# Kernel optimization log

Hardware: AMD Instinct MI355X
Metric: run time of the kernel (lower is better)

Reference implementation:

```python
import jax, jax.numpy as jnp
import numpy as np

B, N, F, C, K = 4, 8192, 128, 64, 16


def setup_inputs() -> dict:
    key = jax.random.key(0)
    ks = jax.random.split(key, 24)
    s = 0.05
    rn = lambda k, shape: (jax.random.normal(k, shape, jnp.float32) * s)
    return {
        "features": jax.random.normal(ks[0], (B, N, F), jnp.float32),
        "positions": jax.random.normal(ks[1], (B, N, 3), jnp.float32),
        "batch": jnp.repeat(jnp.arange(B, dtype=jnp.int32), N),
        "num_neighbors": K,
        # linear encoder (F -> C)
        "W_enc": rn(ks[2], (F, C)), "b_enc": jnp.zeros((C,), jnp.float32),
        # point-transformer q/k/v projections (C -> C)
        "Wq": rn(ks[3], (C, C)), "bq": jnp.zeros((C,), jnp.float32),
        "Wk": rn(ks[4], (C, C)), "bk": jnp.zeros((C,), jnp.float32),
        "Wv": rn(ks[5], (C, C)), "bv": jnp.zeros((C,), jnp.float32),
        # positional encoding MLP: 3 -> C -> C (ReLU)
        "Wp1": rn(ks[6], (3, C)), "bp1": jnp.zeros((C,), jnp.float32),
        "Wp2": rn(ks[7], (C, C)), "bp2": jnp.zeros((C,), jnp.float32),
        # attention MLP gamma: C -> C -> C (ReLU)
        "Wa1": rn(ks[8], (C, C)), "ba1": jnp.zeros((C,), jnp.float32),
        "Wa2": rn(ks[9], (C, C)), "ba2": jnp.zeros((C,), jnp.float32),
        # linear decoder (C -> F)
        "W_dec": rn(ks[10], (C, F)), "b_dec": jnp.zeros((F,), jnp.float32),
    }


def reference(features, positions, batch, num_neighbors,
              W_enc, b_enc, Wq, bq, Wk, bk, Wv, bv,
              Wp1, bp1, Wp2, bp2, Wa1, ba1, Wa2, ba2, W_dec, b_dec):
    # linear encode: [B,N,F] -> [B,N,C]
    x = features @ W_enc + b_enc
    q = x @ Wq + bq
    k = x @ Wk + bk
    v = x @ Wv + bv

    def per_cloud(pos, qi, ki, vi):
        # kNN via pairwise squared distances (self included, dist 0)
        sq = jnp.sum(pos * pos, axis=-1)                      # [N]
        d2 = sq[:, None] + sq[None, :] - 2.0 * (pos @ pos.T)  # [N,N]
        idx = jax.lax.top_k(-d2, num_neighbors)[1]            # [N,K]
        kj = ki[idx]                                          # [N,K,C] gather
        vj = vi[idx]                                          # [N,K,C]
        rel = pos[:, None, :] - pos[idx]                      # [N,K,3]
        # positional encoding delta = MLP(p_i - p_j)
        delta = jax.nn.relu(rel @ Wp1 + bp1) @ Wp2 + bp2      # [N,K,C]
        # vector attention: gamma(q_i - k_j + delta), softmax over K neighbors
        a = qi[:, None, :] - kj + delta
        a = jax.nn.relu(a @ Wa1 + ba1) @ Wa2 + ba2
        w = jax.nn.softmax(a, axis=1)                         # [N,K,C]
        return jnp.sum(w * (vj + delta), axis=1)              # [N,C]

    y = jax.vmap(per_cloud)(positions, q, k, v)               # [B,N,C]
    out = y @ W_dec + b_dec + features                        # decode + residual
    return (out, positions, batch)
```

## Files before the change

### kernel.cpp

```cpp
#include <hip/hip_runtime.h>
#include <hip/hip_bf16.h>

#define NPTS 32768
#define NPC  8192
#define KNN  16
#define CH   64
#define FDIM 128
#define EMPTYKEY 0x7F7FFFFFu

typedef __bf16 bf16;
typedef __bf16 bf16x8 __attribute__((ext_vector_type(8)));
typedef float  f32x4  __attribute__((ext_vector_type(4)));

__global__ __launch_bounds__(256) void k_encode(
    const float* __restrict__ feat,
    const float* __restrict__ Wenc, const float* __restrict__ benc,
    const float* __restrict__ Wq, const float* __restrict__ bq,
    const float* __restrict__ Wk, const float* __restrict__ bk,
    const float* __restrict__ Wv, const float* __restrict__ bv,
    float* __restrict__ qo, float* __restrict__ ko, float* __restrict__ vo)
{
    __shared__ float xs[4][CH];
    int t = threadIdx.x;
    int c = t & 63, pl = t >> 6;
    size_t pt = (size_t)blockIdx.x * 4 + pl;
    const float* fr = feat + pt * FDIM;
    float acc = benc[c];
#pragma unroll 8
    for (int f4 = 0; f4 < 32; ++f4) {
        float4 fv = *reinterpret_cast<const float4*>(fr + f4 * 4);
        acc += fv.x * Wenc[(f4*4+0)*CH + c];
        acc += fv.y * Wenc[(f4*4+1)*CH + c];
        acc += fv.z * Wenc[(f4*4+2)*CH + c];
        acc += fv.w * Wenc[(f4*4+3)*CH + c];
    }
    xs[pl][c] = acc;
    __syncthreads();
    float aq = bq[c], ak = bk[c], av = bv[c];
#pragma unroll 4
    for (int m = 0; m < CH; ++m) {
        float xm = xs[pl][m];
        aq += xm * Wq[m*CH + c];
        ak += xm * Wk[m*CH + c];
        av += xm * Wv[m*CH + c];
    }
    qo[pt*CH + c] = aq; ko[pt*CH + c] = ak; vo[pt*CH + c] = av;
}

__global__ __launch_bounds__(256, 4) void k_knn(
    const float* __restrict__ pos, unsigned* __restrict__ wsK)
{
    __shared__ float4 sp[1024];
    __shared__ unsigned sbuf[256 * 17];

    int t = threadIdx.x;
    int blk = blockIdx.x;
    int slice = blk & 7;
    int qg = (blk >> 3) & 31;
    int cloud = blk >> 8;
    const float* pc = pos + (size_t)cloud * NPC * 3;
    int jbase = slice << 10;

#pragma unroll
    for (int i = 0; i < 4; ++i) {
        int li = t * 4 + i;
        int j = jbase + li;
        sp[li] = make_float4(pc[j*3+0], pc[j*3+1], pc[j*3+2], 0.f);
    }
    __syncthreads();

    int qi = (qg << 8) + t;
    float myx = pc[qi*3+0], myy = pc[qi*3+1], myz = pc[qi*3+2];

    unsigned arr[16];
#pragma unroll
    for (int r = 0; r < 16; ++r) arr[r] = EMPTYKEY;
    float thrf = __uint_as_float(EMPTYKEY & 0xFFFFE000u);
    int cnt = 0;
    int base = t * 17;

    for (int g = 0; g < 1024; g += 4) {
#pragma unroll
        for (int u = 0; u < 4; ++u) {
            float4 p = sp[g + u];
            float dx = myx - p.x, dy = myy - p.y, dz = myz - p.z;
            float d2 = dx*dx + dy*dy + dz*dz;
            unsigned key = (__float_as_uint(d2) & 0xFFFFE000u) | (unsigned)(jbase + g + u);
            sbuf[base + cnt] = key;
            cnt += (d2 <= thrf) ? 1 : 0;
        }
        if (__any(cnt >= 13)) {
#pragma unroll
            for (int b = 0; b < 16; ++b) {
                unsigned key = (b < cnt) ? sbuf[base + b] : EMPTYKEY;
#pragma unroll
                for (int r = 0; r < 16; ++r) {
                    unsigned lo = key < arr[r] ? key : arr[r];
                    unsigned hi = key < arr[r] ? arr[r] : key;
                    arr[r] = lo; key = hi;
                }
            }
            cnt = 0;
            thrf = __uint_as_float(arr[15] & 0xFFFFE000u);
        }
    }
#pragma unroll
    for (int b = 0; b < 16; ++b) {
        unsigned key = (b < cnt) ? sbuf[base + b] : EMPTYKEY;
#pragma unroll
        for (int r = 0; r < 16; ++r) {
            unsigned lo = key < arr[r] ? key : arr[r];
            unsigned hi = key < arr[r] ? arr[r] : key;
            arr[r] = lo; key = hi;
        }
    }
    unsigned* o = wsK + (((size_t)(cloud * NPC + qi)) * 8 + slice) * 16;
#pragma unroll
    for (int r = 0; r < 16; ++r) o[r] = arr[r];
}

__global__ __launch_bounds__(64) void k_merge(
    const unsigned* __restrict__ wsK, int* __restrict__ idxout)
{
    __shared__ unsigned kk[64][137];
    int t = threadIdx.x;
    size_t q = (size_t)blockIdx.x * 64 + t;
    const uint4* src = reinterpret_cast<const uint4*>(wsK + q * 128);
#pragma unroll
    for (int i = 0; i < 32; ++i) {
        uint4 v = src[i];
        int w = i * 4;
        int s = (w >> 4) * 17 + (w & 15);
        kk[t][s] = v.x; kk[t][s+1] = v.y; kk[t][s+2] = v.z; kk[t][s+3] = v.w;
    }
#pragma unroll
    for (int l = 0; l < 8; ++l) kk[t][l*17 + 16] = 0xFFFFFFFFu;

    unsigned h0=0,h1=0,h2=0,h3=0,h4=0,h5=0,h6=0,h7=0;
    int* o = idxout + q * KNN;
    for (int r = 0; r < KNN; ++r) {
        unsigned best = 0xFFFFFFFFu; int bl = 0; unsigned k;
        k = kk[t][0*17 + h0]; if (k < best) { best = k; bl = 0; }
        k = kk[t][1*17 + h1]; if (k < best) { best = k; bl = 1; }
        k = kk[t][2*17 + h2]; if (k < best) { best = k; bl = 2; }
        k = kk[t][3*17 + h3]; if (k < best) { best = k; bl = 3; }
        k = kk[t][4*17 + h4]; if (k < best) { best = k; bl = 4; }
        k = kk[t][5*17 + h5]; if (k < best) { best = k; bl = 5; }
        k = kk[t][6*17 + h6]; if (k < best) { best = k; bl = 6; }
        k = kk[t][7*17 + h7]; if (k < best) { best = k; bl = 7; }
        o[r] = (int)(best & 0x1FFFu);
        h0 += (bl == 0); h1 += (bl == 1); h2 += (bl == 2); h3 += (bl == 3);
        h4 += (bl == 4); h5 += (bl == 5); h6 += (bl == 6); h7 += (bl == 7);
    }
}

__device__ __forceinline__ void wave_gemm(
    const bf16* At, f32x4 acc[4][4], const float* __restrict__ Wg,
    int w, int mlane, int kgrp)
{
    bf16x8 wf[4][2];
#pragma unroll
    for (int nt = 0; nt < 4; ++nt) {
#pragma unroll
        for (int kt = 0; kt < 2; ++kt) {
            bf16x8 v;
#pragma unroll
            for (int j = 0; j < 8; ++j)
                v[j] = (bf16)Wg[(kt*32 + kgrp*8 + j)*CH + nt*16 + mlane];
            wf[nt][kt] = v;
        }
    }
#pragma unroll
    for (int mt = 0; mt < 4; ++mt) {
        int row = w*64 + mt*16 + mlane;
        const bf16* rb = At + row*CH;
        int sw = row & 7;
        bf16x8 a0 = *reinterpret_cast<const bf16x8*>(rb + ((kgrp     ^ sw) * 8));
        bf16x8 a1 = *reinterpret_cast<const bf16x8*>(rb + (((4+kgrp) ^ sw) * 8));
#pragma unroll
        for (int nt = 0; nt < 4; ++nt) {
            acc[mt][nt] = __builtin_amdgcn_mfma_f32_16x16x32_bf16(a0, wf[nt][0], acc[mt][nt], 0, 0, 0);
            acc[mt][nt] = __builtin_amdgcn_mfma_f32_16x16x32_bf16(a1, wf[nt][1], acc[mt][nt], 0, 0, 0);
        }
    }
}

__global__ __launch_bounds__(128) void k_attn(
    const float* __restrict__ pos, const int* __restrict__ nidx,
    const float* __restrict__ qg, const float* __restrict__ kg, const float* __restrict__ vg,
    const float* __restrict__ Wp1, const float* __restrict__ bp1,
    const float* __restrict__ Wp2, const float* __restrict__ bp2,
    const float* __restrict__ Wa1, const float* __restrict__ ba1,
    const float* __restrict__ Wa2, const float* __restrict__ ba2,
    float* __restrict__ yout)
{
    __shared__ bf16 At[128 * CH];
    __shared__ bf16 Vt[128 * CH];

    int t = threadIdx.x;
    int w = t >> 6, lane = t & 63;
    int mlane = lane & 15, kgrp = lane >> 4;
    size_t p0 = (size_t)blockIdx.x * 8;
    size_t cbase = (p0 >> 13) << 13;

    {
        int p = t >> 4, j = t & 15;
        size_t gp = p0 + p;
        int nbr = nidx[gp*KNN + j];
        size_t gn = cbase + (size_t)nbr;
        float rx = pos[gp*3+0] - pos[gn*3+0];
        float ry = pos[gp*3+1] - pos[gn*3+1];
        float rz = pos[gp*3+2] - pos[gn*3+2];
        float h[CH];
#pragma unroll
        for (int c4 = 0; c4 < 16; ++c4) {
            float4 w0 = *reinterpret_cast<const float4*>(Wp1 + 0*CH + c4*4);
            float4 w1 = *reinterpret_cast<const float4*>(Wp1 + 1*CH + c4*4);
            float4 w2 = *reinterpret_cast<const float4*>(Wp1 + 2*CH + c4*4);
            float4 bb = *reinterpret_cast<const float4*>(bp1 + c4*4);
            h[c4*4+0] = fmaxf(rx*w0.x + ry*w1.x + rz*w2.x + bb.x, 0.f);
            h[c4*4+1] = fmaxf(rx*w0.y + ry*w1.y + rz*w2.y + bb.y, 0.f);
            h[c4*4+2] = fmaxf(rx*w0.z + ry*w1.z + rz*w2.z + bb.z, 0.f);
            h[c4*4+3] = fmaxf(rx*w0.w + ry*w1.w + rz*w2.w + bb.w, 0.f);
        }
#pragma unroll
        for (int ch = 0; ch < 8; ++ch) {
            bf16x8 v;
#pragma unroll
            for (int e = 0; e < 8; ++e) v[e] = (bf16)h[ch*8 + e];
            *reinterpret_cast<bf16x8*>(&At[t*CH + (ch ^ (t & 7)) * 8]) = v;
        }
    }

    f32x4 acc[4][4];

#pragma unroll
    for (int nt = 0; nt < 4; ++nt) {
        float b = bp2[nt*16 + mlane];
#pragma unroll
        for (int mt = 0; mt < 4; ++mt) { acc[mt][nt][0]=b; acc[mt][nt][1]=b; acc[mt][nt][2]=b; acc[mt][nt][3]=b; }
    }
    wave_gemm(At, acc, Wp2, w, mlane, kgrp);

#pragma unroll
    for (int mt = 0; mt < 4; ++mt) {
        size_t gp = p0 + (size_t)(w*4 + mt);
        int nb[4];
#pragma unroll
        for (int reg = 0; reg < 4; ++reg)
            nb[reg] = nidx[gp*KNN + kgrp*4 + reg];
#pragma unroll
        for (int nt = 0; nt < 4; ++nt) {
            int c = nt*16 + mlane;
            float qv = qg[gp*CH + c];
#pragma unroll
            for (int reg = 0; reg < 4; ++reg) {
                float dlt = acc[mt][nt][reg];
                size_t gr = cbase + (size_t)nb[reg];
                float kv = kg[gr*CH + c];
                float vv = vg[gr*CH + c];
                int row = w*64 + mt*16 + kgrp*4 + reg;
                int off = row*CH + (((c >> 3) ^ (row & 7)) * 8) + (c & 7);
                At[off] = (bf16)(qv - kv + dlt);
                Vt[off] = (bf16)(vv + dlt);
            }
        }
    }

#pragma unroll
    for (int nt = 0; nt < 4; ++nt) {
        float b = ba1[nt*16 + mlane];
#pragma unroll
        for (int mt = 0; mt < 4; ++mt) { acc[mt][nt][0]=b; acc[mt][nt][1]=b; acc[mt][nt][2]=b; acc[mt][nt][3]=b; }
    }
    wave_gemm(At, acc, Wa1, w, mlane, kgrp);
#pragma unroll
    for (int mt = 0; mt < 4; ++mt) {
#pragma unroll
        for (int nt = 0; nt < 4; ++nt) {
            int c = nt*16 + mlane;
#pragma unroll
            for (int reg = 0; reg < 4; ++reg) {
                int row = w*64 + mt*16 + kgrp*4 + reg;
                int off = row*CH + (((c >> 3) ^ (row & 7)) * 8) + (c & 7);
                At[off] = (bf16)fmaxf(acc[mt][nt][reg], 0.f);
            }
        }
    }

#pragma unroll
    for (int nt = 0; nt < 4; ++nt) {
        float b = ba2[nt*16 + mlane];
#pragma unroll
        for (int mt = 0; mt < 4; ++mt) { acc[mt][nt][0]=b; acc[mt][nt][1]=b; acc[mt][nt][2]=b; acc[mt][nt][3]=b; }
    }
    wave_gemm(At, acc, Wa2, w, mlane, kgrp);

#pragma unroll
    for (int mt = 0; mt < 4; ++mt) {
        size_t gp = p0 + (size_t)(w*4 + mt);
#pragma unroll
        for (int nt = 0; nt < 4; ++nt) {
            int c = nt*16 + mlane;
            float m = fmaxf(fmaxf(acc[mt][nt][0], acc[mt][nt][1]),
                            fmaxf(acc[mt][nt][2], acc[mt][nt][3]));
            m = fmaxf(m, __shfl_xor(m, 16));
            m = fmaxf(m, __shfl_xor(m, 32));
            float e[4], s = 0.f;
#pragma unroll
            for (int reg = 0; reg < 4; ++reg) { e[reg] = __expf(acc[mt][nt][reg] - m); s += e[reg]; }
            s += __shfl_xor(s, 16);
            s += __shfl_xor(s, 32);
            float num = 0.f;
#pragma unroll
            for (int reg = 0; reg < 4; ++reg) {
                int row = w*64 + mt*16 + kgrp*4 + reg;
                int off = row*CH + (((c >> 3) ^ (row & 7)) * 8) + (c & 7);
                num += e[reg] * (float)Vt[off];
            }
            num += __shfl_xor(num, 16);
            num += __shfl_xor(num, 32);
            if (kgrp == 0) yout[gp*CH + c] = num / s;
        }
    }
}

__global__ __launch_bounds__(256) void k_decode(
    const float* __restrict__ y, const float* __restrict__ Wd, const float* __restrict__ bd,
    const float* __restrict__ feat, float* __restrict__ out)
{
    int t = threadIdx.x;
    int f = t & 127, pl = t >> 7;
    size_t pt = (size_t)blockIdx.x * 2 + pl;
    const float* yr = y + pt*CH;
    float acc = bd[f] + feat[pt*FDIM + f];
#pragma unroll
    for (int c4 = 0; c4 < 16; ++c4) {
        float4 yv = *reinterpret_cast<const float4*>(yr + c4*4);
        acc += yv.x * Wd[(c4*4+0)*FDIM + f];
        acc += yv.y * Wd[(c4*4+1)*FDIM + f];
        acc += yv.z * Wd[(c4*4+2)*FDIM + f];
        acc += yv.w * Wd[(c4*4+3)*FDIM + f];
    }
    out[pt*FDIM + f] = acc;
}

__global__ void k_tail(const float* __restrict__ pos, const int* __restrict__ batch,
                       float* __restrict__ outtail)
{
    int i = blockIdx.x * 256 + threadIdx.x;
    if (i < NPTS*3) outtail[i] = pos[i];
    if (i < NPTS)   outtail[NPTS*3 + i] = (float)batch[i];
}

extern "C" void kernel_launch(void* const* d_in, const int* in_sizes, int n_in,
                              void* d_out, int out_size, void* d_ws, size_t ws_size,
                              hipStream_t stream)
{
    const float* feat  = (const float*)d_in[0];
    const float* pos   = (const float*)d_in[1];
    const int*   batch = (const int*)d_in[2];
    const float* Wenc  = (const float*)d_in[4];
    const float* benc  = (const float*)d_in[5];
    const float* Wq = (const float*)d_in[6];   const float* bq = (const float*)d_in[7];
    const float* Wk = (const float*)d_in[8];   const float* bk = (const float*)d_in[9];
    const float* Wv = (const float*)d_in[10];  const float* bv = (const float*)d_in[11];
    const float* Wp1= (const float*)d_in[12];  const float* bp1= (const float*)d_in[13];
    const float* Wp2= (const float*)d_in[14];  const float* bp2= (const float*)d_in[15];
    const float* Wa1= (const float*)d_in[16];  const float* ba1= (const float*)d_in[17];
    const float* Wa2= (const float*)d_in[18];  const float* ba2= (const float*)d_in[19];
    const float* Wd = (const float*)d_in[20];  const float* bd = (const float*)d_in[21];
    float* out = (float*)d_out;

    int*      idx = (int*)d_ws;
    unsigned* wsK = (unsigned*)((char*)d_ws + (size_t)NPTS*KNN*sizeof(int));
    float* qb = (float*)wsK;
    float* kb = qb + (size_t)NPTS*CH;
    float* vb = kb + (size_t)NPTS*CH;
    float* yb = vb + (size_t)NPTS*CH;

    k_knn<<<1024, 256, 0, stream>>>(pos, wsK);
    k_merge<<<NPTS/64, 64, 0, stream>>>(wsK, idx);

    k_encode<<<NPTS/4, 256, 0, stream>>>(feat, Wenc, benc, Wq, bq, Wk, bk, Wv, bv, qb, kb, vb);

    k_attn<<<NPTS/8, 128, 0, stream>>>(pos, idx, qb, kb, vb,
                                       Wp1, bp1, Wp2, bp2, Wa1, ba1, Wa2, ba2, yb);

    k_decode<<<NPTS/2, 256, 0, stream>>>(yb, Wd, bd, feat, out);

    k_tail<<<(NPTS*3 + 255)/256, 256, 0, stream>>>(pos, batch, out + (size_t)NPTS*FDIM);
}
```

Before: 472.6 us.

## Skip kNN candidate writes for distant groups and prepack MFMA weights

In the kNN kernel, the four distances of a group are computed first, and the shared-buffer write and insertion sort only run when some lane has a candidate under the current threshold. This removes the per-point unconditional LDS store. Position loads into shared memory now use vectorized float4 reads. A new tiny k_pack kernel converts Wp2, Wa1 and Wa2 once into MFMA-ready bf16x8 fragments, so each attention block loads 8 vectors instead of doing 64 strided fp32 loads and conversions per GEMM. The cost is one extra launch and more branching in the kNN loop.

```diff
diff --git a/kernel.cpp b/kernel.cpp
--- a/kernel.cpp
+++ b/kernel.cpp
@@ -61,11 +61,13 @@
     const float* pc = pos + (size_t)cloud * NPC * 3;
     int jbase = slice << 10;
 
-#pragma unroll
-    for (int i = 0; i < 4; ++i) {
-        int li = t * 4 + i;
-        int j = jbase + li;
-        sp[li] = make_float4(pc[j*3+0], pc[j*3+1], pc[j*3+2], 0.f);
+    {
+        const float4* src = reinterpret_cast<const float4*>(pc + (size_t)jbase * 3);
+        float4 a = src[t*3+0], b1 = src[t*3+1], c1 = src[t*3+2];
+        sp[t*4+0] = make_float4(a.x,  a.y,  a.z,  0.f);
+        sp[t*4+1] = make_float4(a.w,  b1.x, b1.y, 0.f);
+        sp[t*4+2] = make_float4(b1.z, b1.w, c1.x, 0.f);
+        sp[t*4+3] = make_float4(c1.y, c1.z, c1.w, 0.f);
     }
     __syncthreads();
 
@@ -80,28 +82,37 @@
     int base = t * 17;
 
     for (int g = 0; g < 1024; g += 4) {
+        float d2v[4];
 #pragma unroll
         for (int u = 0; u < 4; ++u) {
             float4 p = sp[g + u];
             float dx = myx - p.x, dy = myy - p.y, dz = myz - p.z;
-            float d2 = dx*dx + dy*dy + dz*dz;
-            unsigned key = (__float_as_uint(d2) & 0xFFFFE000u) | (unsigned)(jbase + g + u);
-            sbuf[base + cnt] = key;
-            cnt += (d2 <= thrf) ? 1 : 0;
-        }
-        if (__any(cnt >= 13)) {
-#pragma unroll
-            for (int b = 0; b < 16; ++b) {
-                unsigned key = (b < cnt) ? sbuf[base + b] : EMPTYKEY;
-#pragma unroll
-                for (int r = 0; r < 16; ++r) {
-                    unsigned lo = key < arr[r] ? key : arr[r];
-                    unsigned hi = key < arr[r] ? arr[r] : key;
-                    arr[r] = lo; key = hi;
+            d2v[u] = dx*dx + dy*dy + dz*dz;
+        }
+        float m4 = fminf(fminf(d2v[0], d2v[1]), fminf(d2v[2], d2v[3]));
+        if (__any(m4 <= thrf)) {
+#pragma unroll
+            for (int u = 0; u < 4; ++u) {
+                if (d2v[u] <= thrf) {
+                    sbuf[base + cnt] = (__float_as_uint(d2v[u]) & 0xFFFFE000u)
+                                       | (unsigned)(jbase + g + u);
+                    ++cnt;
                 }
             }
-            cnt = 0;
-            thrf = __uint_as_float(arr[15] & 0xFFFFE000u);
+            if (__any(cnt >= 13)) {
+#pragma unroll
+                for (int b = 0; b < 16; ++b) {
+                    unsigned key = (b < cnt) ? sbuf[base + b] : EMPTYKEY;
+#pragma unroll
+                    for (int r = 0; r < 16; ++r) {
+                        unsigned lo = min(key, arr[r]);
+                        unsigned hi = max(key, arr[r]);
+                        arr[r] = lo; key = hi;
+                    }
+                }
+                cnt = 0;
+                thrf = __uint_as_float(arr[15] & 0xFFFFE000u);
+            }
         }
     }
 #pragma unroll
@@ -109,8 +120,8 @@
         unsigned key = (b < cnt) ? sbuf[base + b] : EMPTYKEY;
 #pragma unroll
         for (int r = 0; r < 16; ++r) {
-            unsigned lo = key < arr[r] ? key : arr[r];
-            unsigned hi = key < arr[r] ? arr[r] : key;
+            unsigned lo = min(key, arr[r]);
+            unsigned hi = max(key, arr[r]);
             arr[r] = lo; key = hi;
         }
     }
@@ -154,25 +165,43 @@
     }
 }
 
+__global__ __launch_bounds__(64) void k_pack(
+    const float* __restrict__ Wp2, const float* __restrict__ Wa1,
+    const float* __restrict__ Wa2, bf16* __restrict__ wpk)
+{
+    int lane = threadIdx.x;
+    int mlane = lane & 15, kgrp = lane >> 4;
+    const float* Ws[3] = {Wp2, Wa1, Wa2};
+    bf16x8* o = reinterpret_cast<bf16x8*>(wpk);
+    for (int gmm = 0; gmm < 3; ++gmm) {
+#pragma unroll
+        for (int nt = 0; nt < 4; ++nt) {
+#pragma unroll
+            for (int kt = 0; kt < 2; ++kt) {
+                bf16x8 v;
+#pragma unroll
+                for (int j = 0; j < 8; ++j)
+                    v[j] = (bf16)Ws[gmm][(kt*32 + kgrp*8 + j)*CH + nt*16 + mlane];
+                o[(gmm*8 + nt*2 + kt)*64 + lane] = v;
+            }
+        }
+    }
+}
+
 __device__ __forceinline__ void wave_gemm(
-    const bf16* At, f32x4 acc[4][4], const float* __restrict__ Wg,
-    int w, int mlane, int kgrp)
-{
+    const bf16* At, f32x4 acc[4][4], const bf16x8* __restrict__ wpk,
+    int w, int lane)
+{
+    int kgrp = lane >> 4;
     bf16x8 wf[4][2];
 #pragma unroll
-    for (int nt = 0; nt < 4; ++nt) {
-#pragma unroll
-        for (int kt = 0; kt < 2; ++kt) {
-            bf16x8 v;
-#pragma unroll
-            for (int j = 0; j < 8; ++j)
-                v[j] = (bf16)Wg[(kt*32 + kgrp*8 + j)*CH + nt*16 + mlane];
-            wf[nt][kt] = v;
-        }
-    }
+    for (int nt = 0; nt < 4; ++nt)
+#pragma unroll
+        for (int kt = 0; kt < 2; ++kt)
+            wf[nt][kt] = wpk[(nt*2 + kt)*64 + lane];
 #pragma unroll
     for (int mt = 0; mt < 4; ++mt) {
-        int row = w*64 + mt*16 + mlane;
+        int row = w*64 + mt*16 + (lane & 15);
         const bf16* rb = At + row*CH;
         int sw = row & 7;
         bf16x8 a0 = *reinterpret_cast<const bf16x8*>(rb + ((kgrp     ^ sw) * 8));
@@ -189,9 +218,8 @@
     const float* __restrict__ pos, const int* __restrict__ nidx,
     const float* __restrict__ qg, const float* __restrict__ kg, const float* __restrict__ vg,
     const float* __restrict__ Wp1, const float* __restrict__ bp1,
-    const float* __restrict__ Wp2, const float* __restrict__ bp2,
-    const float* __restrict__ Wa1, const float* __restrict__ ba1,
-    const float* __restrict__ Wa2, const float* __restrict__ ba2,
+    const float* __restrict__ bp2, const float* __restrict__ ba1,
+    const float* __restrict__ ba2, const bf16* __restrict__ wpkg,
     float* __restrict__ yout)
 {
     __shared__ bf16 At[128 * CH];
@@ -202,6 +230,7 @@
     int mlane = lane & 15, kgrp = lane >> 4;
     size_t p0 = (size_t)blockIdx.x * 8;
     size_t cbase = (p0 >> 13) << 13;
+    const bf16x8* wpk = reinterpret_cast<const bf16x8*>(wpkg);
 
     {
         int p = t >> 4, j = t & 15;
@@ -240,7 +269,7 @@
 #pragma unroll
         for (int mt = 0; mt < 4; ++mt) { acc[mt][nt][0]=b; acc[mt][nt][1]=b; acc[mt][nt][2]=b; acc[mt][nt][3]=b; }
     }
-    wave_gemm(At, acc, Wp2, w, mlane, kgrp);
+    wave_gemm(At, acc, wpk, w, lane);
 
 #pragma unroll
     for (int mt = 0; mt < 4; ++mt) {
@@ -273,7 +302,7 @@
 #pragma unroll
         for (int mt = 0; mt < 4; ++mt) { acc[mt][nt][0]=b; acc[mt][nt][1]=b; acc[mt][nt][2]=b; acc[mt][nt][3]=b; }
     }
-    wave_gemm(At, acc, Wa1, w, mlane, kgrp);
+    wave_gemm(At, acc, wpk + 512, w, lane);
 #pragma unroll
     for (int mt = 0; mt < 4; ++mt) {
 #pragma unroll
@@ -294,7 +323,7 @@
 #pragma unroll
         for (int mt = 0; mt < 4; ++mt) { acc[mt][nt][0]=b; acc[mt][nt][1]=b; acc[mt][nt][2]=b; acc[mt][nt][3]=b; }
     }
-    wave_gemm(At, acc, Wa2, w, mlane, kgrp);
+    wave_gemm(At, acc, wpk + 1024, w, lane);
 
 #pragma unroll
     for (int mt = 0; mt < 4; ++mt) {
@@ -378,14 +407,16 @@
     float* kb = qb + (size_t)NPTS*CH;
     float* vb = kb + (size_t)NPTS*CH;
     float* yb = vb + (size_t)NPTS*CH;
+    bf16*  wpk = (bf16*)(yb + (size_t)NPTS*CH);
 
     k_knn<<<1024, 256, 0, stream>>>(pos, wsK);
     k_merge<<<NPTS/64, 64, 0, stream>>>(wsK, idx);
+    k_pack<<<1, 64, 0, stream>>>(Wp2, Wa1, Wa2, wpk);
 
     k_encode<<<NPTS/4, 256, 0, stream>>>(feat, Wenc, benc, Wq, bq, Wk, bk, Wv, bv, qb, kb, vb);
 
     k_attn<<<NPTS/8, 128, 0, stream>>>(pos, idx, qb, kb, vb,
-                                       Wp1, bp1, Wp2, bp2, Wa1, ba1, Wa2, ba2, yb);
+                                       Wp1, bp1, bp2, ba1, ba2, wpk, yb);
 
     k_decode<<<NPTS/2, 256, 0, stream>>>(yb, Wd, bd, feat, out);
 
```

New measurement: 466.4 us. About the same (-1.3%).
